# Kernel tuning notes

Hardware: AMD Instinct MI355X
Metric: run time of the kernel (lower is better)

Reference implementation:

```python
import jax, jax.numpy as jnp
import numpy as np
import math

N_HEADS = 4
GROUPS = 32
EPS = 1e-5


def group_norm(x, w, b, groups=GROUPS):
    B, C, H, W = x.shape
    xg = x.reshape(B, groups, C // groups, H, W)
    mu = xg.mean(axis=(2, 3, 4), keepdims=True)
    var = xg.var(axis=(2, 3, 4), keepdims=True)
    xn = ((xg - mu) / jnp.sqrt(var + EPS)).reshape(B, C, H, W)
    return xn * w[None, :, None, None] + b[None, :, None, None]


def setup_inputs() -> dict:
    key = jax.random.key(0)
    ks = jax.random.split(key, 8)
    B, C, H, W = 4, 256, 64, 64
    s = 1.0 / math.sqrt(C)
    return {
        "x": jax.random.normal(ks[0], (B, C, H, W), jnp.float32),
        "context": jax.random.normal(ks[1], (B, C, H, W), jnp.float32),
        "gn_q_w": jnp.ones((C,), jnp.float32),
        "gn_q_b": jnp.zeros((C,), jnp.float32),
        "gn_ctx_w": jnp.ones((C,), jnp.float32),
        "gn_ctx_b": jnp.zeros((C,), jnp.float32),
        "Wq": jax.random.normal(ks[2], (C, C), jnp.float32) * s,
        "Wk": jax.random.normal(ks[3], (C, C), jnp.float32) * s,
        "Wv": jax.random.normal(ks[4], (C, C), jnp.float32) * s,
        "Wo": jax.random.normal(ks[5], (C, C), jnp.float32) * s,
        "bo": jnp.zeros((C,), jnp.float32),
    }


def reference(x, context, gn_q_w, gn_q_b, gn_ctx_w, gn_ctx_b, Wq, Wk, Wv, Wo, bo):
    B, C, H, W = x.shape
    hd = C // N_HEADS
    # 1x1 convs == channel matmuls
    q = jnp.einsum('oc,bchw->bohw', Wq, group_norm(x, gn_q_w, gn_q_b))
    k = jnp.einsum('oc,bchw->bohw', Wk, group_norm(context, gn_ctx_w, gn_ctx_b))
    v = jnp.einsum('oc,bchw->bohw', Wv, context)
    q = q.reshape(B, N_HEADS, hd, H * W)
    k = k.reshape(B, N_HEADS, hd, H * W)
    v = v.reshape(B, N_HEADS, hd, H * W)
    attn = jnp.einsum('bncd,bnce->bnde', q, k) / math.sqrt(hd)  # [B,n,HW,HW]
    attn = jax.nn.softmax(attn, axis=-1)
    out = jnp.einsum('bnde,bnce->bncd', attn, v).reshape(B, C, H, W)
    out = jnp.einsum('oc,bchw->bohw', Wo, out) + bo[None, :, None, None]
    return x + out
```

## Files before the change

kernel.cpp:

```cpp
#include <hip/hip_runtime.h>

typedef __bf16 bf16x8 __attribute__((ext_vector_type(8)));
typedef __bf16 bf16x2 __attribute__((ext_vector_type(2)));
typedef float f32x2 __attribute__((ext_vector_type(2)));
typedef float f32x4 __attribute__((ext_vector_type(4)));
typedef float f32x16 __attribute__((ext_vector_type(16)));

#define DEV static __device__ __forceinline__

DEV unsigned short f2bf(float f) {
  union { float f; unsigned int u; } v; v.f = f;
  unsigned int u = v.u;
  return (unsigned short)((u + 0x7FFFu + ((u >> 16) & 1u)) >> 16);
}

DEV bf16x8 ldb8(const unsigned short* p) { return *reinterpret_cast<const bf16x8*>(p); }

DEV bf16x8 ldsb8(const unsigned short* base, int byteoff) {
  return *reinterpret_cast<const bf16x8*>((const char*)base + byteoff);
}

DEV f32x4 mfma(bf16x8 a, bf16x8 b, f32x4 c) {
  return __builtin_amdgcn_mfma_f32_16x16x32_bf16(a, b, c, 0, 0, 0);
}
DEV f32x16 mfma32(bf16x8 a, bf16x8 b, f32x16 c) {
  return __builtin_amdgcn_mfma_f32_32x32x16_bf16(a, b, c, 0, 0, 0);
}

DEV float fexp2(float x) {
  float r;
  asm("v_exp_f32 %0, %1" : "=v"(r) : "v"(x));
  return r;
}

DEV unsigned cvtpk(float a, float b) {
  f32x2 t = {a, b};
  bf16x2 r = __builtin_convertvector(t, bf16x2);
  return __builtin_bit_cast(unsigned, r);
}

DEV bf16x8 pack4(unsigned w0, unsigned w1, unsigned w2, unsigned w3) {
  union { unsigned u[4]; bf16x8 v; } x;
  x.u[0] = w0; x.u[1] = w1; x.u[2] = w2; x.u[3] = w3;
  return x.v;
}

DEV f32x16 zero16() {
  f32x16 z;
#pragma unroll
  for (int i = 0; i < 16; ++i) z[i] = 0.f;
  return z;
}

__global__ __launch_bounds__(256) void gn_stats_kernel(
    const float* __restrict__ x, const float* __restrict__ ctx,
    const float* __restrict__ gqw, const float* __restrict__ gqb,
    const float* __restrict__ gcw, const float* __restrict__ gcb,
    float* __restrict__ ssbuf) {
  int id = blockIdx.x;
  int tensor = id >> 7;
  int bg = id & 127;
  int b = bg >> 5, g = bg & 31;
  const float* src = tensor ? ctx : x;
  const float* gw = tensor ? gcw : gqw;
  const float* gb = tensor ? gcb : gqb;
  float* scale = ssbuf + tensor * 2048;
  float* shift = scale + 1024;

  const float* base = src + (size_t)(b * 256 + g * 8) * 4096;
  int tid = threadIdx.x;
  float s = 0.f, sq = 0.f;
#pragma unroll
  for (int i = 0; i < 32; ++i) {
    float4 v = *reinterpret_cast<const float4*>(base + (i * 256 + tid) * 4);
    s += v.x + v.y + v.z + v.w;
    sq += v.x * v.x + v.y * v.y + v.z * v.z + v.w * v.w;
  }
#pragma unroll
  for (int sh = 32; sh; sh >>= 1) {
    s += __shfl_down(s, sh);
    sq += __shfl_down(sq, sh);
  }
  __shared__ float rs[4], rq[4], mr[2];
  int w = tid >> 6;
  if ((tid & 63) == 0) { rs[w] = s; rq[w] = sq; }
  __syncthreads();
  if (tid == 0) {
    float S = rs[0] + rs[1] + rs[2] + rs[3];
    float Q = rq[0] + rq[1] + rq[2] + rq[3];
    float mean = S * (1.f / 32768.f);
    float var = Q * (1.f / 32768.f) - mean * mean;
    mr[0] = mean;
    mr[1] = rsqrtf(var + 1e-5f);
  }
  __syncthreads();
  if (tid < 8) {
    int c = g * 8 + tid;
    float sc = gw[c] * mr[1];
    scale[b * 256 + c] = sc;
    shift[b * 256 + c] = gb[c] - mr[0] * sc;
  }
}

template <int OUTMODE>
__global__ __launch_bounds__(256) void proj_kernel(
    const float* __restrict__ W, const float* __restrict__ in,
    const float* __restrict__ scale, const float* __restrict__ shift,
    unsigned short* __restrict__ out, float wscale) {
  __shared__ unsigned short Alds[128][72];
  __shared__ unsigned short Blds[128][72];
  const int b = blockIdx.z;
  const int o0 = blockIdx.y * 128;
  const int p0 = blockIdx.x * 128;
  const int tid = threadIdx.x;
  const int w = tid >> 6, lane = tid & 63;
  const int g = lane >> 4, l15 = lane & 15;
  const int oh = (w >> 1) * 64, ph = (w & 1) * 64;

  f32x4 acc[4][4];
#pragma unroll
  for (int i = 0; i < 4; ++i)
#pragma unroll
    for (int j = 0; j < 4; ++j) acc[i][j] = (f32x4){0.f, 0.f, 0.f, 0.f};

  for (int kk = 0; kk < 4; ++kk) {
    const int c0 = kk * 64;
    __syncthreads();
#pragma unroll
    for (int i = 0; i < 8; ++i) {
      int idx = i * 256 + tid;
      int row = idx >> 4, col4 = (idx & 15) * 4;
      float4 wv = *reinterpret_cast<const float4*>(&W[(size_t)(o0 + row) * 256 + c0 + col4]);
      ushort4 bv = {f2bf(wv.x * wscale), f2bf(wv.y * wscale),
                    f2bf(wv.z * wscale), f2bf(wv.w * wscale)};
      *reinterpret_cast<ushort4*>(&Alds[row][col4]) = bv;
    }
#pragma unroll
    for (int i = 0; i < 8; ++i) {
      int idx = i * 256 + tid;
      int cc = idx >> 5, p4 = (idx & 31) * 4;
      int c = c0 + cc;
      float4 xv = *reinterpret_cast<const float4*>(&in[((size_t)b * 256 + c) * 4096 + p0 + p4]);
      float sc = 1.f, sh = 0.f;
      if (scale) { sc = scale[b * 256 + c]; sh = shift[b * 256 + c]; }
      Blds[p4 + 0][cc] = f2bf(xv.x * sc + sh);
      Blds[p4 + 1][cc] = f2bf(xv.y * sc + sh);
      Blds[p4 + 2][cc] = f2bf(xv.z * sc + sh);
      Blds[p4 + 3][cc] = f2bf(xv.w * sc + sh);
    }
    __syncthreads();
#pragma unroll
    for (int kf = 0; kf < 2; ++kf) {
      bf16x8 av[4], bv[4];
#pragma unroll
      for (int mf = 0; mf < 4; ++mf) av[mf] = ldb8(&Alds[oh + mf * 16 + l15][kf * 32 + g * 8]);
#pragma unroll
      for (int nf = 0; nf < 4; ++nf) bv[nf] = ldb8(&Blds[ph + nf * 16 + l15][kf * 32 + g * 8]);
#pragma unroll
      for (int mf = 0; mf < 4; ++mf)
#pragma unroll
        for (int nf = 0; nf < 4; ++nf) acc[mf][nf] = mfma(av[mf], bv[nf], acc[mf][nf]);
    }
  }
#pragma unroll
  for (int mf = 0; mf < 4; ++mf)
#pragma unroll
    for (int nf = 0; nf < 4; ++nf) {
      int o = o0 + oh + mf * 16 + g * 4;
      int p = p0 + ph + nf * 16 + l15;
      if (OUTMODE == 0) {
        int h = o >> 6, ch = o & 63;
        ushort4 vv = {f2bf(acc[mf][nf][0]), f2bf(acc[mf][nf][1]),
                      f2bf(acc[mf][nf][2]), f2bf(acc[mf][nf][3])};
        *reinterpret_cast<ushort4*>(&out[(((size_t)b * 4 + h) * 4096 + p) * 64 + ch]) = vv;
      } else {
#pragma unroll
        for (int r = 0; r < 4; ++r) {
          int oo = o + r;
          out[(((size_t)b * 4 + (oo >> 6)) * 64 + (oo & 63)) * 4096 + p] = f2bf(acc[mf][nf][r]);
        }
      }
    }
}

DEV void stageK(const unsigned short* kg, int t, char* ldsbase, int tidg) {
#pragma unroll
  for (int i = 0; i < 2; ++i) {
    int o = i * 4096 + tidg * 16;
    int r = o >> 7;
    int col = (o & 127) ^ ((r & 7) << 4);
    const char* src = (const char*)(kg + (size_t)(t * 64 + r) * 64) + col;
    __builtin_amdgcn_global_load_lds(
        (__attribute__((address_space(1))) void*)src,
        (__attribute__((address_space(3))) void*)(ldsbase + i * 4096 + (tidg >> 6) * 1024),
        16, 0, 0);
  }
}

DEV void stageV(const unsigned short* vg, int t, char* ldsbase, int tidg) {
#pragma unroll
  for (int i = 0; i < 2; ++i) {
    int o = i * 4096 + tidg * 16;
    int r = o >> 7;
    int col = (o & 127) ^ ((r & 7) << 4);
    const char* src = (const char*)(vg + (size_t)r * 4096 + t * 64) + col;
    __builtin_amdgcn_global_load_lds(
        (__attribute__((address_space(1))) void*)src,
        (__attribute__((address_space(3))) void*)(ldsbase + i * 4096 + (tidg >> 6) * 1024),
        16, 0, 0);
  }
}

__global__ __launch_bounds__(512) void attn_kernel(
    const unsigned short* __restrict__ QT, const unsigned short* __restrict__ KT,
    const unsigned short* __restrict__ V, unsigned short* __restrict__ OT) {
  __shared__ __align__(16) char smem[65536];
  const int bh = blockIdx.x;
  const int tid = threadIdx.x;
  const int w = tid >> 6, lane = tid & 63;
  const int g = w >> 2, wl = w & 3;
  const int tidg = tid & 255;
  const int hi = lane >> 5, l31 = lane & 31;
  const int d = blockIdx.y * 128 + wl * 32 + l31;

  char* Kb[2] = {smem + (g * 2 + 0) * 8192, smem + (g * 2 + 1) * 8192};
  char* Vb[2] = {smem + 32768 + (g * 2 + 0) * 8192, smem + 32768 + (g * 2 + 1) * 8192};

  const unsigned short* kg = KT + (size_t)bh * 4096 * 64;
  const unsigned short* vg = V + (size_t)bh * 64 * 4096;

  bf16x8 q[4];
#pragma unroll
  for (int ks = 0; ks < 4; ++ks)
    q[ks] = ldb8(&QT[((size_t)bh * 4096 + d) * 64 + ks * 16 + hi * 8]);

  f32x16 oacc[2];
  oacc[0] = zero16();
  oacc[1] = zero16();
  float lsum = 0.f;
  const int swz = (l31 & 7) << 4;
  const int t0 = g * 32;

  auto compute = [&](const char* kb_, const char* vb_) {
    const unsigned short* kb = (const unsigned short*)kb_;
    const unsigned short* vb = (const unsigned short*)vb_;
    f32x16 st[2];
    st[0] = zero16();
    st[1] = zero16();
    __builtin_amdgcn_s_setprio(1);
#pragma unroll
    for (int ks = 0; ks < 4; ++ks) {
      bf16x8 k0 = ldsb8(kb, l31 * 128 + ((ks * 32 + hi * 16) ^ swz));
      bf16x8 k1 = ldsb8(kb, (32 + l31) * 128 + ((ks * 32 + hi * 16) ^ swz));
      st[0] = mfma32(k0, q[ks], st[0]);
      st[1] = mfma32(k1, q[ks], st[1]);
    }
    __builtin_amdgcn_s_setprio(0);

#pragma unroll
    for (int eb = 0; eb < 2; ++eb)
#pragma unroll
      for (int i = 0; i < 16; ++i) st[eb][i] = fexp2(st[eb][i]);
    float ss[16];
#pragma unroll
    for (int i = 0; i < 16; ++i) ss[i] = st[0][i] + st[1][i];
#pragma unroll
    for (int s2 = 8; s2 > 0; s2 >>= 1)
#pragma unroll
      for (int i = 0; i < s2; ++i) ss[i] += ss[i + s2];
    lsum += ss[0] + __shfl_xor(ss[0], 32);

#pragma unroll
    for (int eb = 0; eb < 2; ++eb)
#pragma unroll
      for (int sh = 0; sh < 2; ++sh) {
        const int rb = sh * 8;
        unsigned a0 = cvtpk(st[eb][rb + 0], st[eb][rb + 1]);
        unsigned b0 = cvtpk(st[eb][rb + 4], st[eb][rb + 5]);
        unsigned a1 = cvtpk(st[eb][rb + 2], st[eb][rb + 3]);
        unsigned b1 = cvtpk(st[eb][rb + 6], st[eb][rb + 7]);
        auto r0 = __builtin_amdgcn_permlane32_swap(a0, b0, false, false);
        auto r1 = __builtin_amdgcn_permlane32_swap(a1, b1, false, false);
        bf16x8 pf = pack4(r0[0], r1[0], r0[1], r1[1]);
        const int s = eb * 2 + sh;
        bf16x8 v0 = ldsb8(vb, l31 * 128 + ((s * 32 + hi * 16) ^ swz));
        bf16x8 v1 = ldsb8(vb, (32 + l31) * 128 + ((s * 32 + hi * 16) ^ swz));
        __builtin_amdgcn_s_setprio(1);
        oacc[0] = mfma32(v0, pf, oacc[0]);
        oacc[1] = mfma32(v1, pf, oacc[1]);
        __builtin_amdgcn_s_setprio(0);
      }
  };

  stageK(kg, t0, Kb[0], tidg);
  stageV(vg, t0, Vb[0], tidg);
  __syncthreads();

  for (int t2 = 0; t2 < 16; ++t2) {
    const int tt = t0 + t2 * 2;
    stageK(kg, tt + 1, Kb[1], tidg);
    stageV(vg, tt + 1, Vb[1], tidg);
    compute(Kb[0], Vb[0]);
    __syncthreads();
    if (t2 < 15) {
      stageK(kg, tt + 2, Kb[0], tidg);
      stageV(vg, tt + 2, Vb[0], tidg);
    }
    compute(Kb[1], Vb[1]);
    __syncthreads();
  }

  float* combO = (float*)smem;
  float* combL = (float*)(smem + 33792);
  float* slot = combO + (wl * 64 + lane) * 33;
  if (g == 1) {
#pragma unroll
    for (int i = 0; i < 16; ++i) { slot[i] = oacc[0][i]; slot[16 + i] = oacc[1][i]; }
    combL[wl * 64 + lane] = lsum;
  }
  __syncthreads();
  if (g == 0) {
#pragma unroll
    for (int i = 0; i < 16; ++i) { oacc[0][i] += slot[i]; oacc[1][i] += slot[16 + i]; }
    lsum += combL[wl * 64 + lane];
    float inv = 1.f / lsum;
    size_t obase = ((size_t)bh * 4096 + d) * 64;
#pragma unroll
    for (int cb = 0; cb < 2; ++cb)
#pragma unroll
      for (int gq = 0; gq < 4; ++gq) {
        ushort4 sv;
        sv.x = f2bf(oacc[cb][gq * 4 + 0] * inv);
        sv.y = f2bf(oacc[cb][gq * 4 + 1] * inv);
        sv.z = f2bf(oacc[cb][gq * 4 + 2] * inv);
        sv.w = f2bf(oacc[cb][gq * 4 + 3] * inv);
        *reinterpret_cast<ushort4*>(&OT[obase + cb * 32 + gq * 8 + hi * 4]) = sv;
      }
  }
}

__global__ __launch_bounds__(256) void final_kernel(
    const float* __restrict__ Wo, const unsigned short* __restrict__ OT,
    const float* __restrict__ bo, const float* __restrict__ x,
    float* __restrict__ out) {
  __shared__ unsigned short Alds[128][72];
  __shared__ unsigned short Blds[128][72];
  const int b = blockIdx.z;
  const int o0 = blockIdx.y * 128;
  const int p0 = blockIdx.x * 128;
  const int tid = threadIdx.x;
  const int w = tid >> 6, lane = tid & 63;
  const int g = lane >> 4, l15 = lane & 15;
  const int oh = (w >> 1) * 64, ph = (w & 1) * 64;

  f32x4 acc[4][4];
#pragma unroll
  for (int i = 0; i < 4; ++i)
#pragma unroll
    for (int j = 0; j < 4; ++j) acc[i][j] = (f32x4){0.f, 0.f, 0.f, 0.f};

  for (int kk = 0; kk < 4; ++kk) {
    const int c0 = kk * 64;
    __syncthreads();
#pragma unroll
    for (int i = 0; i < 8; ++i) {
      int idx = i * 256 + tid;
      int row = idx >> 4, col4 = (idx & 15) * 4;
      float4 wv = *reinterpret_cast<const float4*>(&Wo[(size_t)(o0 + row) * 256 + c0 + col4]);
      ushort4 bv = {f2bf(wv.x), f2bf(wv.y), f2bf(wv.z), f2bf(wv.w)};
      *reinterpret_cast<ushort4*>(&Alds[row][col4]) = bv;
    }
#pragma unroll
    for (int i = 0; i < 4; ++i) {
      int idx = i * 256 + tid;
      int row = idx >> 3, c8 = (idx & 7) * 8;
      *reinterpret_cast<uint4*>(&Blds[row][c8]) =
          *reinterpret_cast<const uint4*>(&OT[(((size_t)b * 4 + kk) * 4096 + p0 + row) * 64 + c8]);
    }
    __syncthreads();
#pragma unroll
    for (int kf = 0; kf < 2; ++kf) {
      bf16x8 av[4], bv[4];
#pragma unroll
      for (int mf = 0; mf < 4; ++mf) av[mf] = ldb8(&Alds[oh + mf * 16 + l15][kf * 32 + g * 8]);
#pragma unroll
      for (int nf = 0; nf < 4; ++nf) bv[nf] = ldb8(&Blds[ph + nf * 16 + l15][kf * 32 + g * 8]);
#pragma unroll
      for (int mf = 0; mf < 4; ++mf)
#pragma unroll
        for (int nf = 0; nf < 4; ++nf) acc[mf][nf] = mfma(av[mf], bv[nf], acc[mf][nf]);
    }
  }
#pragma unroll
  for (int mf = 0; mf < 4; ++mf)
#pragma unroll
    for (int nf = 0; nf < 4; ++nf) {
      int o = o0 + oh + mf * 16 + g * 4;
      int p = p0 + ph + nf * 16 + l15;
#pragma unroll
      for (int r = 0; r < 4; ++r) {
        size_t idx = ((size_t)b * 256 + o + r) * 4096 + p;
        out[idx] = acc[mf][nf][r] + bo[o + r] + x[idx];
      }
    }
}

extern "C" void kernel_launch(void* const* d_in, const int* in_sizes, int n_in,
                              void* d_out, int out_size, void* d_ws, size_t ws_size,
                              hipStream_t stream) {
  const float* x = (const float*)d_in[0];
  const float* ctx = (const float*)d_in[1];
  const float* gqw = (const float*)d_in[2];
  const float* gqb = (const float*)d_in[3];
  const float* gcw = (const float*)d_in[4];
  const float* gcb = (const float*)d_in[5];
  const float* Wq = (const float*)d_in[6];
  const float* Wk = (const float*)d_in[7];
  const float* Wv = (const float*)d_in[8];
  const float* Wo = (const float*)d_in[9];
  const float* bo = (const float*)d_in[10];
  float* out = (float*)d_out;

  char* ws = (char*)d_ws;
  float* ssbuf = (float*)ws;
  float* scaleQ = ssbuf;
  float* shiftQ = ssbuf + 1024;
  float* scaleK = ssbuf + 2048;
  float* shiftK = ssbuf + 3072;
  const size_t TEN = (size_t)4 * 4 * 4096 * 64;
  unsigned short* QT = (unsigned short*)(ws + 65536);
  unsigned short* KT = QT + TEN;
  unsigned short* Vb = KT + TEN;
  unsigned short* OT = Vb + TEN;

  gn_stats_kernel<<<256, 256, 0, stream>>>(x, ctx, gqw, gqb, gcw, gcb, ssbuf);

  const float beta = 0.125f * 1.44269504088896340736f;
  dim3 pg(32, 2, 4);
  proj_kernel<0><<<pg, 256, 0, stream>>>(Wq, x, scaleQ, shiftQ, QT, beta);
  proj_kernel<0><<<pg, 256, 0, stream>>>(Wk, ctx, scaleK, shiftK, KT, 1.f);
  proj_kernel<1><<<pg, 256, 0, stream>>>(Wv, ctx, nullptr, nullptr, Vb, 1.f);

  attn_kernel<<<dim3(16, 32), 512, 0, stream>>>(QT, KT, Vb, OT);

  final_kernel<<<pg, 256, 0, stream>>>(Wo, OT, bo, x, out);
}
```

Before: 153.3 us.

## Drop LDS staging in projection GEMMs and load V fragments directly to registers

```diff
diff --git a/kernel.cpp b/kernel.cpp
--- a/kernel.cpp
+++ b/kernel.cpp
@@ -107,8 +107,6 @@
     const float* __restrict__ W, const float* __restrict__ in,
     const float* __restrict__ scale, const float* __restrict__ shift,
     unsigned short* __restrict__ out, float wscale) {
-  __shared__ unsigned short Alds[128][72];
-  __shared__ unsigned short Blds[128][72];
   const int b = blockIdx.z;
   const int o0 = blockIdx.y * 128;
   const int p0 = blockIdx.x * 128;
@@ -124,42 +122,41 @@
     for (int j = 0; j < 4; ++j) acc[i][j] = (f32x4){0.f, 0.f, 0.f, 0.f};
 
   for (int kk = 0; kk < 4; ++kk) {
-    const int c0 = kk * 64;
-    __syncthreads();
-#pragma unroll
-    for (int i = 0; i < 8; ++i) {
-      int idx = i * 256 + tid;
-      int row = idx >> 4, col4 = (idx & 15) * 4;
-      float4 wv = *reinterpret_cast<const float4*>(&W[(size_t)(o0 + row) * 256 + c0 + col4]);
-      ushort4 bv = {f2bf(wv.x * wscale), f2bf(wv.y * wscale),
-                    f2bf(wv.z * wscale), f2bf(wv.w * wscale)};
-      *reinterpret_cast<ushort4*>(&Alds[row][col4]) = bv;
-    }
-#pragma unroll
-    for (int i = 0; i < 8; ++i) {
-      int idx = i * 256 + tid;
-      int cc = idx >> 5, p4 = (idx & 31) * 4;
-      int c = c0 + cc;
-      float4 xv = *reinterpret_cast<const float4*>(&in[((size_t)b * 256 + c) * 4096 + p0 + p4]);
-      float sc = 1.f, sh = 0.f;
-      if (scale) { sc = scale[b * 256 + c]; sh = shift[b * 256 + c]; }
-      Blds[p4 + 0][cc] = f2bf(xv.x * sc + sh);
-      Blds[p4 + 1][cc] = f2bf(xv.y * sc + sh);
-      Blds[p4 + 2][cc] = f2bf(xv.z * sc + sh);
-      Blds[p4 + 3][cc] = f2bf(xv.w * sc + sh);
-    }
-    __syncthreads();
 #pragma unroll
     for (int kf = 0; kf < 2; ++kf) {
+      const int cb = kk * 64 + kf * 32 + g * 8;
+      float sc8[8], sh8[8];
+#pragma unroll
+      for (int j = 0; j < 8; ++j) {
+        sc8[j] = scale ? scale[b * 256 + cb + j] : 1.f;
+        sh8[j] = shift ? shift[b * 256 + cb + j] : 0.f;
+      }
       bf16x8 av[4], bv[4];
 #pragma unroll
-      for (int mf = 0; mf < 4; ++mf) av[mf] = ldb8(&Alds[oh + mf * 16 + l15][kf * 32 + g * 8]);
-#pragma unroll
-      for (int nf = 0; nf < 4; ++nf) bv[nf] = ldb8(&Blds[ph + nf * 16 + l15][kf * 32 + g * 8]);
+      for (int mf = 0; mf < 4; ++mf) {
+        const float* wp = &W[(size_t)(o0 + oh + mf * 16 + l15) * 256 + cb];
+        float4 w0 = *reinterpret_cast<const float4*>(wp);
+        float4 w1 = *reinterpret_cast<const float4*>(wp + 4);
+        av[mf] = pack4(cvtpk(w0.x * wscale, w0.y * wscale),
+                       cvtpk(w0.z * wscale, w0.w * wscale),
+                       cvtpk(w1.x * wscale, w1.y * wscale),
+                       cvtpk(w1.z * wscale, w1.w * wscale));
+      }
+#pragma unroll
+      for (int nf = 0; nf < 4; ++nf) {
+        const int p = p0 + ph + nf * 16 + l15;
+        float v[8];
+#pragma unroll
+        for (int j = 0; j < 8; ++j)
+          v[j] = in[((size_t)b * 256 + cb + j) * 4096 + p] * sc8[j] + sh8[j];
+        bv[nf] = pack4(cvtpk(v[0], v[1]), cvtpk(v[2], v[3]),
+                       cvtpk(v[4], v[5]), cvtpk(v[6], v[7]));
+      }
 #pragma unroll
       for (int mf = 0; mf < 4; ++mf)
 #pragma unroll
-        for (int nf = 0; nf < 4; ++nf) acc[mf][nf] = mfma(av[mf], bv[nf], acc[mf][nf]);
+        for (int nf = 0; nf < 4; ++nf)
+          acc[mf][nf] = mfma(av[mf], bv[nf], acc[mf][nf]);
     }
   }
 #pragma unroll
@@ -197,24 +194,19 @@
   }
 }
 
-DEV void stageV(const unsigned short* vg, int t, char* ldsbase, int tidg) {
-#pragma unroll
-  for (int i = 0; i < 2; ++i) {
-    int o = i * 4096 + tidg * 16;
-    int r = o >> 7;
-    int col = (o & 127) ^ ((r & 7) << 4);
-    const char* src = (const char*)(vg + (size_t)r * 4096 + t * 64) + col;
-    __builtin_amdgcn_global_load_lds(
-        (__attribute__((address_space(1))) void*)src,
-        (__attribute__((address_space(3))) void*)(ldsbase + i * 4096 + (tidg >> 6) * 1024),
-        16, 0, 0);
-  }
+DEV void loadV(const unsigned short* vg, int t, bf16x8 (&vf)[2][4], int hi, int l31) {
+  const unsigned short* vt = vg + t * 64;
+#pragma unroll
+  for (int half = 0; half < 2; ++half)
+#pragma unroll
+    for (int s = 0; s < 4; ++s)
+      vf[half][s] = ldb8(&vt[(size_t)(half * 32 + l31) * 4096 + s * 16 + hi * 8]);
 }
 
 __global__ __launch_bounds__(512) void attn_kernel(
     const unsigned short* __restrict__ QT, const unsigned short* __restrict__ KT,
     const unsigned short* __restrict__ V, unsigned short* __restrict__ OT) {
-  __shared__ __align__(16) char smem[65536];
+  __shared__ __align__(16) char smem[34816];
   const int bh = blockIdx.x;
   const int tid = threadIdx.x;
   const int w = tid >> 6, lane = tid & 63;
@@ -223,8 +215,8 @@
   const int hi = lane >> 5, l31 = lane & 31;
   const int d = blockIdx.y * 128 + wl * 32 + l31;
 
-  char* Kb[2] = {smem + (g * 2 + 0) * 8192, smem + (g * 2 + 1) * 8192};
-  char* Vb[2] = {smem + 32768 + (g * 2 + 0) * 8192, smem + 32768 + (g * 2 + 1) * 8192};
+  char* Kb0 = smem + g * 16384;
+  char* Kb1 = Kb0 + 8192;
 
   const unsigned short* kg = KT + (size_t)bh * 4096 * 64;
   const unsigned short* vg = V + (size_t)bh * 64 * 4096;
@@ -241,9 +233,8 @@
   const int swz = (l31 & 7) << 4;
   const int t0 = g * 32;
 
-  auto compute = [&](const char* kb_, const char* vb_) {
+  auto compute = [&](const char* kb_, const bf16x8 (&vf)[2][4]) {
     const unsigned short* kb = (const unsigned short*)kb_;
-    const unsigned short* vb = (const unsigned short*)vb_;
     f32x16 st[2];
     st[0] = zero16();
     st[1] = zero16();
@@ -261,15 +252,18 @@
     for (int eb = 0; eb < 2; ++eb)
 #pragma unroll
       for (int i = 0; i < 16; ++i) st[eb][i] = fexp2(st[eb][i]);
-    float ss[16];
-#pragma unroll
-    for (int i = 0; i < 16; ++i) ss[i] = st[0][i] + st[1][i];
-#pragma unroll
-    for (int s2 = 8; s2 > 0; s2 >>= 1)
+
+    float ss[8];
+#pragma unroll
+    for (int i = 0; i < 8; ++i)
+      ss[i] = (st[0][i] + st[0][i + 8]) + (st[1][i] + st[1][i + 8]);
+#pragma unroll
+    for (int s2 = 4; s2 > 0; s2 >>= 1)
 #pragma unroll
       for (int i = 0; i < s2; ++i) ss[i] += ss[i + s2];
     lsum += ss[0] + __shfl_xor(ss[0], 32);
 
+    bf16x8 pf[4];
 #pragma unroll
     for (int eb = 0; eb < 2; ++eb)
 #pragma unroll
@@ -281,32 +275,32 @@
         unsigned b1 = cvtpk(st[eb][rb + 6], st[eb][rb + 7]);
         auto r0 = __builtin_amdgcn_permlane32_swap(a0, b0, false, false);
         auto r1 = __builtin_amdgcn_permlane32_swap(a1, b1, false, false);
-        bf16x8 pf = pack4(r0[0], r1[0], r0[1], r1[1]);
-        const int s = eb * 2 + sh;
-        bf16x8 v0 = ldsb8(vb, l31 * 128 + ((s * 32 + hi * 16) ^ swz));
-        bf16x8 v1 = ldsb8(vb, (32 + l31) * 128 + ((s * 32 + hi * 16) ^ swz));
-        __builtin_amdgcn_s_setprio(1);
-        oacc[0] = mfma32(v0, pf, oacc[0]);
-        oacc[1] = mfma32(v1, pf, oacc[1]);
-        __builtin_amdgcn_s_setprio(0);
-      }
+        pf[eb * 2 + sh] = pack4(r0[0], r1[0], r0[1], r1[1]);
+      }
+#pragma unroll
+    for (int s = 0; s < 4; ++s) {
+      __builtin_amdgcn_s_setprio(1);
+      oacc[0] = mfma32(vf[0][s], pf[s], oacc[0]);
+      oacc[1] = mfma32(vf[1][s], pf[s], oacc[1]);
+      __builtin_amdgcn_s_setprio(0);
+    }
   };
 
-  stageK(kg, t0, Kb[0], tidg);
-  stageV(vg, t0, Vb[0], tidg);
+  bf16x8 vf[2][4];
+  stageK(kg, t0, Kb0, tidg);
   __syncthreads();
 
   for (int t2 = 0; t2 < 16; ++t2) {
     const int tt = t0 + t2 * 2;
-    stageK(kg, tt + 1, Kb[1], tidg);
-    stageV(vg, tt + 1, Vb[1], tidg);
-    compute(Kb[0], Vb[0]);
+    loadV(vg, tt, vf, hi, l31);
+    __builtin_amdgcn_sched_barrier(0);
+    stageK(kg, tt + 1, Kb1, tidg);
+    compute(Kb0, vf);
     __syncthreads();
-    if (t2 < 15) {
-      stageK(kg, tt + 2, Kb[0], tidg);
-      stageV(vg, tt + 2, Vb[0], tidg);
-    }
-    compute(Kb[1], Vb[1]);
+    loadV(vg, tt + 1, vf, hi, l31);
+    __builtin_amdgcn_sched_barrier(0);
+    if (t2 < 15) stageK(kg, tt + 2, Kb0, tidg);
+    compute(Kb1, vf);
     __syncthreads();
   }
 
@@ -343,8 +337,6 @@
     const float* __restrict__ Wo, const unsigned short* __restrict__ OT,
     const float* __restrict__ bo, const float* __restrict__ x,
     float* __restrict__ out) {
-  __shared__ unsigned short Alds[128][72];
-  __shared__ unsigned short Blds[128][72];
   const int b = blockIdx.z;
   const int o0 = blockIdx.y * 128;
   const int p0 = blockIdx.x * 128;
@@ -360,35 +352,28 @@
     for (int j = 0; j < 4; ++j) acc[i][j] = (f32x4){0.f, 0.f, 0.f, 0.f};
 
   for (int kk = 0; kk < 4; ++kk) {
-    const int c0 = kk * 64;
-    __syncthreads();
-#pragma unroll
-    for (int i = 0; i < 8; ++i) {
-      int idx = i * 256 + tid;
-      int row = idx >> 4, col4 = (idx & 15) * 4;
-      float4 wv = *reinterpret_cast<const float4*>(&Wo[(size_t)(o0 + row) * 256 + c0 + col4]);
-      ushort4 bv = {f2bf(wv.x), f2bf(wv.y), f2bf(wv.z), f2bf(wv.w)};
-      *reinterpret_cast<ushort4*>(&Alds[row][col4]) = bv;
-    }
-#pragma unroll
-    for (int i = 0; i < 4; ++i) {
-      int idx = i * 256 + tid;
-      int row = idx >> 3, c8 = (idx & 7) * 8;
-      *reinterpret_cast<uint4*>(&Blds[row][c8]) =
-          *reinterpret_cast<const uint4*>(&OT[(((size_t)b * 4 + kk) * 4096 + p0 + row) * 64 + c8]);
-    }
-    __syncthreads();
 #pragma unroll
     for (int kf = 0; kf < 2; ++kf) {
+      const int cb = kf * 32 + g * 8;
       bf16x8 av[4], bv[4];
 #pragma unroll
-      for (int mf = 0; mf < 4; ++mf) av[mf] = ldb8(&Alds[oh + mf * 16 + l15][kf * 32 + g * 8]);
-#pragma unroll
-      for (int nf = 0; nf < 4; ++nf) bv[nf] = ldb8(&Blds[ph + nf * 16 + l15][kf * 32 + g * 8]);
+      for (int mf = 0; mf < 4; ++mf) {
+        const float* wp = &Wo[(size_t)(o0 + oh + mf * 16 + l15) * 256 + kk * 64 + cb];
+        float4 w0 = *reinterpret_cast<const float4*>(wp);
+        float4 w1 = *reinterpret_cast<const float4*>(wp + 4);
+        av[mf] = pack4(cvtpk(w0.x, w0.y), cvtpk(w0.z, w0.w),
+                       cvtpk(w1.x, w1.y), cvtpk(w1.z, w1.w));
+      }
+#pragma unroll
+      for (int nf = 0; nf < 4; ++nf) {
+        const int p = p0 + ph + nf * 16 + l15;
+        bv[nf] = ldb8(&OT[(((size_t)b * 4 + kk) * 4096 + p) * 64 + cb]);
+      }
 #pragma unroll
       for (int mf = 0; mf < 4; ++mf)
 #pragma unroll
-        for (int nf = 0; nf < 4; ++nf) acc[mf][nf] = mfma(av[mf], bv[nf], acc[mf][nf]);
+        for (int nf = 0; nf < 4; ++nf)
+          acc[mf][nf] = mfma(av[mf], bv[nf], acc[mf][nf]);
     }
   }
 #pragma unroll
```

New measurement: 220.6 us. 1.44x slower.
